# Optimization experiments

Hardware: AMD Instinct MI355X
Metric: run time of the kernel (lower is better)

## Reference

```python
import jax, jax.numpy as jnp
import numpy as np

N, C, T, V = 16, 128, 128, 25
K, H, OC = 3, 8, 256          # kernel_size subsets, heads, out_channels
HOPMAX = 12                   # hop values in [0, 12); emb_table size HOPMAX
EPS_BN = 1e-5
EPS_NORM = 1e-4


def setup_inputs() -> dict:
    key = jax.random.key(0)
    ks = jax.random.split(key, 12)
    s = 0.05
    x = jax.random.normal(ks[0], (N, C, T, V), jnp.float32)
    hop = jax.random.randint(ks[1], (V, V), 0, HOPMAX)
    emb_table = jax.random.normal(ks[2], (K, H, HOPMAX), jnp.float32) * s
    # A initialized as identity (as in the module) plus small noise for nontrivial grads
    A = jnp.tile(jnp.eye(V, dtype=jnp.float32), (K, H, 1, 1)) \
        + jax.random.normal(ks[3], (K, H, V, V), jnp.float32) * s
    w_block = jax.random.normal(ks[4], (K * OC, C // H), jnp.float32) * s  # grouped 1x1 conv, groups=K*H
    b_block = jax.random.normal(ks[5], (K * OC,), jnp.float32) * s
    bn_gamma = jnp.ones((OC,), jnp.float32)
    bn_beta = jnp.zeros((OC,), jnp.float32)
    res_w = jax.random.normal(ks[6], (OC, C), jnp.float32) * s  # residual 1x1 conv
    res_b = jax.random.normal(ks[7], (OC,), jnp.float32) * s
    res_bn_gamma = jnp.ones((OC,), jnp.float32)
    res_bn_beta = jnp.zeros((OC,), jnp.float32)
    return {"x": x, "hop": hop, "emb_table": emb_table, "A": A,
            "w_block": w_block, "b_block": b_block,
            "bn_gamma": bn_gamma, "bn_beta": bn_beta,
            "res_w": res_w, "res_b": res_b,
            "res_bn_gamma": res_bn_gamma, "res_bn_beta": res_bn_beta}


def _batchnorm(x, gamma, beta):
    # training-mode BatchNorm2d: batch stats over (N, T, V), biased variance
    m = jnp.mean(x, axis=(0, 2, 3), keepdims=True)
    v = jnp.var(x, axis=(0, 2, 3), keepdims=True)
    xn = (x - m) * jax.lax.rsqrt(v + EPS_BN)
    return gamma[None, :, None, None] * xn + beta[None, :, None, None]


def _l2_col_norm(w):
    # torch.norm(w, p=2, dim=-2, keepdim=True) + 1e-4  (in-degree normalization)
    return jnp.sqrt(jnp.sum(w * w, axis=-2, keepdims=True)) + EPS_NORM


def reference(x, hop, emb_table, A, w_block, b_block, bn_gamma, bn_beta,
              res_w, res_b, res_bn_gamma, res_bn_beta):
    n, c, t, v = x.shape
    # residual: 1x1 TemporalConv2d + BN (in_channels != out_channels)
    res = jnp.einsum('nctv,oc->notv', x, res_w) + res_b[None, :, None, None]
    res = _batchnorm(res, res_bn_gamma, res_bn_beta)

    # hop-embedding gather -> [K, H, V, V]; fuse normalized B and A
    B = emb_table[:, :, hop]
    BnA = B / _l2_col_norm(B) + A / _l2_col_norm(A)

    # graph conv: einsum over joint dim v (broadcast over k)
    xh = x.reshape(n, H, c // H, t, v)                      # [N,H,C/H,T,V]
    y = jnp.einsum('nhctv,khvw->nkhctw', xh, BnA)           # [N,K,H,C/H,T,V]
    y = y.reshape(n, K * H, c // H, t, v)                   # groups = K*H

    # grouped 1x1 conv: per-group [C/H -> OC/H] GEMM
    wg = w_block.reshape(K * H, OC // H, c // H)
    out = jnp.einsum('ngctv,goc->ngotv', y, wg)             # [N,K*H,OC/H,T,V]
    out = out.reshape(n, K * OC, t, v) + b_block[None, :, None, None]

    # sum over the K kernel subsets
    out = out.reshape(n, K, OC, t, v).sum(axis=1)
    out = _batchnorm(out, bn_gamma, bn_beta)
    return jax.nn.relu(out + res)
```

## Files before the change

kernel.cpp:

```cpp
#include <hip/hip_runtime.h>
#include <stdint.h>

typedef __attribute__((ext_vector_type(8))) short short8;
typedef __attribute__((ext_vector_type(4))) float f32x4;

#define B_BNA    0ull
#define B_STATS  60416ull
#define B_RESW2  64512ull
#define B_E2     1178624ull
#define B_XB     7994368ull
#define B_MAIN   21625856ull
#define B_RES    47840256ull

#define NTV 51200.0f

__device__ __forceinline__ unsigned short f2bf(float f) {
    unsigned u = __float_as_uint(f);
    return (unsigned short)((u + 0x7fffu + ((u >> 16) & 1u)) >> 16);
}
__device__ __forceinline__ float bf2f(unsigned s) { return __uint_as_float(s << 16); }

__device__ __forceinline__ float wave_sum(float v) {
#pragma unroll
    for (int m = 1; m < 64; m <<= 1) v += __shfl_xor(v, m, 64);
    return v;
}

__device__ __forceinline__ void gl_lds16(const unsigned short* g, unsigned short* l) {
    __builtin_amdgcn_global_load_lds(
        (const __attribute__((address_space(1))) unsigned int*)g,
        (__attribute__((address_space(3))) unsigned int*)l, 16, 0, 0);
}
__device__ __forceinline__ void stage_pair(const unsigned short* g0, const unsigned short* g1,
                                           unsigned short* d) {
    gl_lds16(g0, d);
    gl_lds16(g1, d + 512);
}

__device__ __forceinline__ int swz_idx(int row, int quad) {
    int rowX = row ^ ((row >> 2) & 1);
    return rowX * 32 + ((quad ^ (row & 3)) << 3);
}

__global__ __launch_bounds__(256) void k_prep(const int* __restrict__ hop,
                                              const float* __restrict__ emb,
                                              const float* __restrict__ A,
                                              const float* __restrict__ res_w,
                                              float* __restrict__ bna,
                                              float* __restrict__ stats,
                                              unsigned short* __restrict__ resw2) {
    int g = blockIdx.x, tid = threadIdx.x;
    if (g < 24) {
        if (tid < 25) {
            int w = tid;
            float nb = 0.f, na = 0.f;
            for (int v = 0; v < 25; v++) {
                float e = emb[g*12 + hop[v*25 + w]];
                nb += e*e;
                float a = A[((size_t)g*25 + v)*25 + w];
                na += a*a;
            }
            nb = sqrtf(nb) + 1e-4f;
            na = sqrtf(na) + 1e-4f;
            for (int v = 0; v < 25; v++) {
                float e = emb[g*12 + hop[v*25 + w]];
                float a = A[((size_t)g*25 + v)*25 + w];
                bna[g*625 + v*25 + w] = e/nb + a/na;
            }
        }
    } else if (g == 24) {
#pragma unroll
        for (int i = 0; i < 4; i++) stats[i*256 + tid] = 0.f;
    } else {
        int base = (g - 25) * 4096 + tid * 16;
#pragma unroll
        for (int j = 0; j < 16; j++) resw2[base + j] = f2bf(res_w[base + j]);
    }
}

__global__ __launch_bounds__(256) void k_prep2x(const float* __restrict__ w_block,
                                                const float* __restrict__ bna,
                                                unsigned short* __restrict__ E2,
                                                const float* __restrict__ x,
                                                unsigned short* __restrict__ xb) {
    int bid = blockIdx.x, tid = threadIdx.x;
    if (bid < 128) {
        __shared__ float bl[3*625];
        __shared__ float wl[3*64];
        int half = bid & 1, og = (bid >> 1) & 7, h = bid >> 4;

        for (int i = tid; i < 1875; i += 256) {
            int k3 = i / 625, j = i - k3*625;
            bl[i] = bna[(k3*8 + h)*625 + j];
        }
        if (tid < 192) {
            int k3 = tid >> 6, o = (tid >> 4) & 3, c = tid & 15;
            wl[tid] = w_block[(k3*256 + h*32 + og*4 + o)*16 + c];
        }
        __syncthreads();

        unsigned short* dst = E2 + (size_t)(h*8 + og)*53248;
        int e0 = half * 26624;
        for (int e = e0 + tid; e < e0 + 26624; e += 256) {
            int kc = e >> 12;
            int n  = (e >> 5) & 127;
            int kk = e & 31;
            int k  = kc*32 + kk;
            int o  = n >> 5, w = n & 31;
            float val = 0.f;
            if (k < 400 && w < 25) {
                int c = k / 25, v = k - c*25;
                val = wl[0*64 + o*16 + c] * bl[0*625 + v*25 + w]
                    + wl[1*64 + o*16 + c] * bl[1*625 + v*25 + w]
                    + wl[2*64 + o*16 + c] * bl[2*625 + v*25 + w];
            }
            dst[e] = f2bf(val);
        }
    } else {
        int b = bid - 128;
        int n_ = b >> 7, t_ = b & 127;
        unsigned short* row = xb + (size_t)b * 3328;
        for (int idx = tid; idx < 3200; idx += 256) {
            int c = idx / 25, v = idx - c*25;
            float val = x[(((size_t)n_*128 + c)*128 + t_)*25 + v];
            row[(c >> 4)*416 + (c & 15)*25 + v] = f2bf(val);
        }
        if (tid < 128) row[(tid >> 4)*416 + 400 + (tid & 15)] = 0;
    }
}

__global__ __launch_bounds__(256) void k_mm(const unsigned short* __restrict__ xb,
                                            const unsigned short* __restrict__ E2,
                                            unsigned short* __restrict__ mainp,
                                            const float* __restrict__ x,
                                            const unsigned short* __restrict__ resw2,
                                            unsigned short* __restrict__ resp,
                                            float* __restrict__ stats) {
    __shared__ unsigned short lds[16384];
    int bid = blockIdx.x, tid = threadIdx.x;
    int lane = tid & 63, wave = tid >> 6;
    int wm = wave >> 1, wn = wave & 1;
    int lane15 = lane & 15, quad = lane >> 4;

    int Lrow0 = wave*32 + (lane >> 2), Lq = lane & 3;
    int r0 = Lrow0 ^ ((Lrow0 >> 2) & 1), q0 = Lq ^ (r0 & 3);
    int Lrow1 = Lrow0 + 16;
    int r1 = Lrow1 ^ ((Lrow1 >> 2) & 1), q1 = Lq ^ (r1 & 3);

    unsigned short* Ad = lds        + wave*1024 + lane*8;
    unsigned short* Bd = lds + 4096 + wave*1024 + lane*8;

    if (bid < 1024) {
        int h = bid & 7, og = (bid >> 3) & 7, mt = bid >> 6;

        const unsigned short* agA0 = xb + (size_t)(mt*128 + r0)*3328 + h*416 + q0*8;
        const unsigned short* agA1 = xb + (size_t)(mt*128 + r1)*3328 + h*416 + q1*8;
        const unsigned short* eb   = E2 + (size_t)(h*8 + og)*53248;
        const unsigned short* bgB0 = eb + r0*32 + q0*8;
        const unsigned short* bgB1 = eb + r1*32 + q1*8;

        f32x4 acc[4][4] = {};

        stage_pair(agA0, agA1, Ad);
        stage_pair(bgB0, bgB1, Bd);
        __syncthreads();

        for (int kc = 0; kc < 13; kc++) {
            int cur = (kc & 1) << 13;
            if (kc < 12) {
                int nxt = 8192 - cur;
                stage_pair(agA0 + (kc+1)*32,            agA1 + (kc+1)*32,            Ad + nxt);
                stage_pair(bgB0 + (size_t)(kc+1)*4096,  bgB1 + (size_t)(kc+1)*4096,  Bd + nxt);
                __builtin_amdgcn_sched_barrier(0);
            }
            const unsigned short* Ac = lds + cur;
            const unsigned short* Bc = lds + 4096 + cur;

            short8 af[4], bq[4];
#pragma unroll
            for (int i = 0; i < 4; i++) {
                af[i] = *(const short8*)&Ac[swz_idx(wm*64 + i*16 + lane15, quad)];
                bq[i] = *(const short8*)&Bc[swz_idx(wn*64 + i*16 + lane15, quad)];
            }
#pragma unroll
            for (int i = 0; i < 4; i++)
#pragma unroll
                for (int j = 0; j < 4; j++)
                    acc[i][j] = __builtin_amdgcn_mfma_f32_16x16x32_bf16(af[i], bq[j], acc[i][j], 0, 0, 0);
            if (kc < 12) __syncthreads();
        }

        float s1[2] = {0.f, 0.f}, s2[2] = {0.f, 0.f};
#pragma unroll
        for (int j = 0; j < 4; j++) {
            int w = (j & 1)*16 + lane15;
            int p = j >> 1;
            if (w < 25) {
                int oc = h*32 + og*4 + wn*2 + p;
#pragma unroll
                for (int i = 0; i < 4; i++) {
                    int mb = mt*128 + wm*64 + i*16 + quad*4;
#pragma unroll
                    for (int r = 0; r < 4; r++) {
                        float val = acc[i][j][r];
                        mainp[(size_t)((mb + r)*256 + oc)*25 + w] = f2bf(val);
                        s1[p] += val;
                        s2[p] = fmaf(val, val, s2[p]);
                    }
                }
            }
        }
#pragma unroll
        for (int p = 0; p < 2; p++) {
            float a = wave_sum(s1[p]);
            float b = wave_sum(s2[p]);
            if (lane == 0) {
                int oc = h*32 + og*4 + wn*2 + p;
                atomicAdd(&stats[oc], a);
                atomicAdd(&stats[256 + oc], b);
            }
        }
    } else {
        int b2 = bid - 1024;
        int nt = (b2 >= 400) ? 1 : 0;
        int mt = b2 - nt*400;

        int n  = mt / 25;
        int off = (mt - n*25) * 128;
        const float* xb2 = x + (size_t)n*409600 + off;

        int c2 = tid >> 4, seg = tid & 15;

        const unsigned short* rb0 = resw2 + (size_t)(nt*128 + r0)*128 + q0*8;
        const unsigned short* rb1 = resw2 + (size_t)(nt*128 + r1)*128 + q1*8;

        f32x4 acc[4][4] = {};

        for (int kc = 0; kc < 4; kc++) {
            stage_pair(rb0 + kc*32, rb1 + kc*32, Bd);
            const float* xc0 = xb2 + (size_t)(kc*32 + 2*c2)*3200;
            const float* xc1 = xc0 + 3200;
            int wbase = 2*(c2 & 3), qn = c2 >> 2;
#pragma unroll
            for (int j = 0; j < 8; j++) {
                int m = seg + 16*j;
                unsigned pk = (unsigned)f2bf(xc0[m]) | ((unsigned)f2bf(xc1[m]) << 16);
                *(unsigned*)&lds[swz_idx(m, qn) + wbase] = pk;
            }
            __syncthreads();

            short8 af[4], bq[4];
#pragma unroll
            for (int i = 0; i < 4; i++) {
                af[i] = *(const short8*)&lds[swz_idx(wm*64 + i*16 + lane15, quad)];
                bq[i] = *(const short8*)&lds[4096 + swz_idx(wn*64 + i*16 + lane15, quad)];
            }
#pragma unroll
            for (int i = 0; i < 4; i++)
#pragma unroll
                for (int j = 0; j < 4; j++)
                    acc[i][j] = __builtin_amdgcn_mfma_f32_16x16x32_bf16(af[i], bq[j], acc[i][j], 0, 0, 0);
            __syncthreads();
        }

#pragma unroll
        for (int j = 0; j < 4; j++) {
            int oc = nt*128 + wn*64 + j*16 + lane15;
            float s1 = 0.f, s2 = 0.f;
#pragma unroll
            for (int i = 0; i < 4; i++) {
                int m2b = mt*128 + wm*64 + i*16 + quad*4;
#pragma unroll
                for (int r = 0; r < 4; r++) {
                    float val = acc[i][j][r];
                    int m2e = m2b + r;
                    int b = m2e / 25, v = m2e - b*25;
                    resp[(size_t)(b*256 + oc)*25 + v] = f2bf(val);
                    s1 += val;
                    s2 = fmaf(val, val, s2);
                }
            }
            s1 += __shfl_xor(s1, 16, 64); s1 += __shfl_xor(s1, 32, 64);
            s2 += __shfl_xor(s2, 16, 64); s2 += __shfl_xor(s2, 32, 64);
            if (quad == 0) {
                atomicAdd(&stats[512 + oc], s1);
                atomicAdd(&stats[768 + oc], s2);
            }
        }
    }
}

__global__ __launch_bounds__(256) void k_final(const float* __restrict__ bn_g,
                                               const float* __restrict__ bn_b,
                                               const float* __restrict__ rbn_g,
                                               const float* __restrict__ rbn_b,
                                               const float* __restrict__ stats,
                                               const unsigned short* __restrict__ mainp,
                                               const unsigned short* __restrict__ resp,
                                               float* __restrict__ out) {
    int b = blockIdx.x;
    int n_ = b >> 7, t_ = b & 127;
    int oc = threadIdx.x;
    const float inv = 1.f / NTV;
    float s1 = stats[oc],       s2 = stats[256 + oc];
    float r1 = stats[512 + oc], r2 = stats[768 + oc];
    float mm = s1*inv, vm = s2*inv - mm*mm;
    float mr = r1*inv, vr = r2*inv - mr*mr;
    float a1 = bn_g[oc]  * rsqrtf(vm + 1e-5f); float c1 = bn_b[oc]  - a1*mm;
    float a2 = rbn_g[oc] * rsqrtf(vr + 1e-5f); float c2 = rbn_b[oc] - a2*mr;

    const unsigned short* mrow = mainp + (size_t)(b*256 + oc)*25;
    const unsigned short* rrow = resp  + (size_t)(b*256 + oc)*25;
    float* op = out + ((size_t)(n_*256 + oc)*128 + t_)*25;
#pragma unroll
    for (int w = 0; w < 25; w++) {
        float val = fmaf(a1, bf2f(mrow[w]), c1) + fmaf(a2, bf2f(rrow[w]), c2);
        op[w] = fmaxf(val, 0.f);
    }
}

extern "C" void kernel_launch(void* const* d_in, const int* in_sizes, int n_in,
                              void* d_out, int out_size, void* d_ws, size_t ws_size,
                              hipStream_t stream) {
    const float* x        = (const float*)d_in[0];
    const int*   hop      = (const int*)  d_in[1];
    const float* emb      = (const float*)d_in[2];
    const float* A        = (const float*)d_in[3];
    const float* w_block  = (const float*)d_in[4];
    const float* bn_g     = (const float*)d_in[6];
    const float* bn_b     = (const float*)d_in[7];
    const float* res_w    = (const float*)d_in[8];
    const float* rbn_g    = (const float*)d_in[10];
    const float* rbn_b    = (const float*)d_in[11];
    float* out = (float*)d_out;

    char* ws = (char*)d_ws;
    float*          bna    = (float*)(ws + B_BNA);
    float*          stats  = (float*)(ws + B_STATS);
    unsigned short* resw2  = (unsigned short*)(ws + B_RESW2);
    unsigned short* E2     = (unsigned short*)(ws + B_E2);
    unsigned short* xb     = (unsigned short*)(ws + B_XB);
    unsigned short* mainp  = (unsigned short*)(ws + B_MAIN);
    unsigned short* resp   = (unsigned short*)(ws + B_RES);

    k_prep   <<<33,   256, 0, stream>>>(hop, emb, A, res_w, bna, stats, resw2);
    k_prep2x <<<2176, 256, 0, stream>>>(w_block, bna, E2, x, xb);
    k_mm     <<<1824, 256, 0, stream>>>(xb, E2, mainp, x, resw2, resp, stats);
    k_final  <<<2048, 256, 0, stream>>>(bn_g, bn_b, rbn_g, rbn_b, stats, mainp, resp, out);
}
```

Before: 222.5 us.

## Triple-buffer main GEMM loads and store intermediates in output layout for vectorized epilogue

The main GEMM loop moves from double to triple buffering in LDS. Explicit vmcnt waits and barriers keep two tiles in flight, so fewer global loads stall the MFMA work. The intermediate main and residual buffers are now written in the final NCTV layout. This lets the final BN+ReLU kernel stream contiguous 16-byte bf16 chunks and write float4 outputs instead of doing per-thread scalar 25-element loops. The cost is more LDS per block, which can lower occupancy, plus scattered epilogue stores in the GEMM.

```diff
diff --git a/kernel.cpp b/kernel.cpp
--- a/kernel.cpp
+++ b/kernel.cpp
@@ -136,7 +136,7 @@
                                             const unsigned short* __restrict__ resw2,
                                             unsigned short* __restrict__ resp,
                                             float* __restrict__ stats) {
-    __shared__ unsigned short lds[16384];
+    __shared__ unsigned short lds[24576];
     int bid = blockIdx.x, tid = threadIdx.x;
     int lane = tid & 63, wave = tid >> 6;
     int wm = wave >> 1, wn = wave & 1;
@@ -147,8 +147,7 @@
     int Lrow1 = Lrow0 + 16;
     int r1 = Lrow1 ^ ((Lrow1 >> 2) & 1), q1 = Lq ^ (r1 & 3);
 
-    unsigned short* Ad = lds        + wave*1024 + lane*8;
-    unsigned short* Bd = lds + 4096 + wave*1024 + lane*8;
+    const int adoff = wave*1024 + lane*8;
 
     if (bid < 1024) {
         int h = bid & 7, og = (bid >> 3) & 7, mt = bid >> 6;
@@ -161,33 +160,46 @@
 
         f32x4 acc[4][4] = {};
 
-        stage_pair(agA0, agA1, Ad);
-        stage_pair(bgB0, bgB1, Bd);
-        __syncthreads();
-
+#pragma unroll
+        for (int p = 0; p < 3; p++) {
+            int bo = p*8192;
+            stage_pair(agA0 + p*32,           agA1 + p*32,           lds + bo + adoff);
+            stage_pair(bgB0 + (size_t)p*4096, bgB1 + (size_t)p*4096, lds + bo + 4096 + adoff);
+        }
+
+        int bufo = 0;
         for (int kc = 0; kc < 13; kc++) {
-            int cur = (kc & 1) << 13;
-            if (kc < 12) {
-                int nxt = 8192 - cur;
-                stage_pair(agA0 + (kc+1)*32,            agA1 + (kc+1)*32,            Ad + nxt);
-                stage_pair(bgB0 + (size_t)(kc+1)*4096,  bgB1 + (size_t)(kc+1)*4096,  Bd + nxt);
-                __builtin_amdgcn_sched_barrier(0);
-            }
-            const unsigned short* Ac = lds + cur;
-            const unsigned short* Bc = lds + 4096 + cur;
-
+            if (kc <= 10)      asm volatile("s_waitcnt vmcnt(8)" ::: "memory");
+            else if (kc == 11) asm volatile("s_waitcnt vmcnt(4)" ::: "memory");
+            else               asm volatile("s_waitcnt vmcnt(0)" ::: "memory");
+            __builtin_amdgcn_s_barrier();
+
+            const unsigned short* Ac = lds + bufo;
+            const unsigned short* Bc = lds + bufo + 4096;
             short8 af[4], bq[4];
 #pragma unroll
             for (int i = 0; i < 4; i++) {
                 af[i] = *(const short8*)&Ac[swz_idx(wm*64 + i*16 + lane15, quad)];
                 bq[i] = *(const short8*)&Bc[swz_idx(wn*64 + i*16 + lane15, quad)];
             }
+            asm volatile("s_waitcnt lgkmcnt(0)" ::: "memory");
+            __builtin_amdgcn_sched_barrier(0);
+            __builtin_amdgcn_s_barrier();
+
+            if (kc <= 9) {
+                stage_pair(agA0 + (kc+3)*32,            agA1 + (kc+3)*32,
+                           lds + bufo + adoff);
+                stage_pair(bgB0 + (size_t)(kc+3)*4096,  bgB1 + (size_t)(kc+3)*4096,
+                           lds + bufo + 4096 + adoff);
+            }
 #pragma unroll
             for (int i = 0; i < 4; i++)
 #pragma unroll
                 for (int j = 0; j < 4; j++)
                     acc[i][j] = __builtin_amdgcn_mfma_f32_16x16x32_bf16(af[i], bq[j], acc[i][j], 0, 0, 0);
-            if (kc < 12) __syncthreads();
+
+            bufo += 8192;
+            if (bufo == 24576) bufo = 0;
         }
 
         float s1[2] = {0.f, 0.f}, s2[2] = {0.f, 0.f};
@@ -199,11 +211,11 @@
                 int oc = h*32 + og*4 + wn*2 + p;
 #pragma unroll
                 for (int i = 0; i < 4; i++) {
-                    int mb = mt*128 + wm*64 + i*16 + quad*4;
+                    int tb = wm*64 + i*16 + quad*4;
 #pragma unroll
                     for (int r = 0; r < 4; r++) {
                         float val = acc[i][j][r];
-                        mainp[(size_t)((mb + r)*256 + oc)*25 + w] = f2bf(val);
+                        mainp[((size_t)(mt*256 + oc)*128 + tb + r)*25 + w] = f2bf(val);
                         s1[p] += val;
                         s2[p] = fmaf(val, val, s2[p]);
                     }
@@ -237,7 +249,7 @@
         f32x4 acc[4][4] = {};
 
         for (int kc = 0; kc < 4; kc++) {
-            stage_pair(rb0 + kc*32, rb1 + kc*32, Bd);
+            stage_pair(rb0 + kc*32, rb1 + kc*32, lds + 4096 + adoff);
             const float* xc0 = xb2 + (size_t)(kc*32 + 2*c2)*3200;
             const float* xc1 = xc0 + 3200;
             int wbase = 2*(c2 & 3), qn = c2 >> 2;
@@ -275,7 +287,8 @@
                     float val = acc[i][j][r];
                     int m2e = m2b + r;
                     int b = m2e / 25, v = m2e - b*25;
-                    resp[(size_t)(b*256 + oc)*25 + v] = f2bf(val);
+                    int nn = b >> 7, t = b & 127;
+                    resp[((size_t)(nn*256 + oc)*128 + t)*25 + v] = f2bf(val);
                     s1 += val;
                     s2 = fmaf(val, val, s2);
                 }
@@ -298,24 +311,55 @@
                                                const unsigned short* __restrict__ mainp,
                                                const unsigned short* __restrict__ resp,
                                                float* __restrict__ out) {
-    int b = blockIdx.x;
-    int n_ = b >> 7, t_ = b & 127;
-    int oc = threadIdx.x;
-    const float inv = 1.f / NTV;
-    float s1 = stats[oc],       s2 = stats[256 + oc];
-    float r1 = stats[512 + oc], r2 = stats[768 + oc];
-    float mm = s1*inv, vm = s2*inv - mm*mm;
-    float mr = r1*inv, vr = r2*inv - mr*mr;
-    float a1 = bn_g[oc]  * rsqrtf(vm + 1e-5f); float c1 = bn_b[oc]  - a1*mm;
-    float a2 = rbn_g[oc] * rsqrtf(vr + 1e-5f); float c2 = rbn_b[oc] - a2*mr;
-
-    const unsigned short* mrow = mainp + (size_t)(b*256 + oc)*25;
-    const unsigned short* rrow = resp  + (size_t)(b*256 + oc)*25;
-    float* op = out + ((size_t)(n_*256 + oc)*128 + t_)*25;
-#pragma unroll
-    for (int w = 0; w < 25; w++) {
-        float val = fmaf(a1, bf2f(mrow[w]), c1) + fmaf(a2, bf2f(rrow[w]), c2);
-        op[w] = fmaxf(val, 0.f);
+    __shared__ float4 cf[8];
+    int bid = blockIdx.x, tid = threadIdx.x;
+    int base_row = (bid * 1024) / 400;
+    if (tid < 8) {
+        int row = base_row + tid;
+        if (row < 4096) {
+            int oc = row & 255;
+            const float inv = 1.f / NTV;
+            float s1 = stats[oc],       s2 = stats[256 + oc];
+            float r1v = stats[512 + oc], r2v = stats[768 + oc];
+            float mm = s1*inv, vm = s2*inv - mm*mm;
+            float mr = r1v*inv, vr = r2v*inv - mr*mr;
+            float a1 = bn_g[oc]  * rsqrtf(vm + 1e-5f);
+            float c1 = bn_b[oc]  - a1*mm;
+            float a2 = rbn_g[oc] * rsqrtf(vr + 1e-5f);
+            float c2 = rbn_b[oc] - a2*mr;
+            cf[tid] = make_float4(a1, c1, a2, c2);
+        }
+    }
+    __syncthreads();
+
+    const uint4* m4 = (const uint4*)mainp;
+    const uint4* r4 = (const uint4*)resp;
+    float4* o4 = (float4*)out;
+#pragma unroll
+    for (int r = 0; r < 4; r++) {
+        int chunk = bid*1024 + r*256 + tid;
+        uint4 mu = m4[chunk];
+        uint4 ru = r4[chunk];
+        float4 C = cf[chunk/400 - base_row];
+        float4 f0, f1;
+        f0.x = fmaxf(fmaf(C.x, __uint_as_float(mu.x << 16),        C.y)
+                   + fmaf(C.z, __uint_as_float(ru.x << 16),        C.w), 0.f);
+        f0.y = fmaxf(fmaf(C.x, __uint_as_float(mu.x & 0xffff0000u), C.y)
+                   + fmaf(C.z, __uint_as_float(ru.x & 0xffff0000u), C.w), 0.f);
+        f0.z = fmaxf(fmaf(C.x, __uint_as_float(mu.y << 16),        C.y)
+                   + fmaf(C.z, __uint_as_float(ru.y << 16),        C.w), 0.f);
+        f0.w = fmaxf(fmaf(C.x, __uint_as_float(mu.y & 0xffff0000u), C.y)
+                   + fmaf(C.z, __uint_as_float(ru.y & 0xffff0000u), C.w), 0.f);
+        f1.x = fmaxf(fmaf(C.x, __uint_as_float(mu.z << 16),        C.y)
+                   + fmaf(C.z, __uint_as_float(ru.z << 16),        C.w), 0.f);
+        f1.y = fmaxf(fmaf(C.x, __uint_as_float(mu.z & 0xffff0000u), C.y)
+                   + fmaf(C.z, __uint_as_float(ru.z & 0xffff0000u), C.w), 0.f);
+        f1.z = fmaxf(fmaf(C.x, __uint_as_float(mu.w << 16),        C.y)
+                   + fmaf(C.z, __uint_as_float(ru.w << 16),        C.w), 0.f);
+        f1.w = fmaxf(fmaf(C.x, __uint_as_float(mu.w & 0xffff0000u), C.y)
+                   + fmaf(C.z, __uint_as_float(ru.w & 0xffff0000u), C.w), 0.f);
+        o4[chunk*2]     = f0;
+        o4[chunk*2 + 1] = f1;
     }
 }
 
@@ -346,5 +390,5 @@
     k_prep   <<<33,   256, 0, stream>>>(hop, emb, A, res_w, bna, stats, resw2);
     k_prep2x <<<2176, 256, 0, stream>>>(w_block, bna, E2, x, xb);
     k_mm     <<<1824, 256, 0, stream>>>(xb, E2, mainp, x, resw2, resp, stats);
-    k_final  <<<2048, 256, 0, stream>>>(bn_g, bn_b, rbn_g, rbn_b, stats, mainp, resp, out);
-}
+    k_final  <<<1600, 256, 0, stream>>>(bn_g, bn_b, rbn_g, rbn_b, stats, mainp, resp, out);
+}
```

Result: faster. 206.3 us (-7.3%).
